# Performance work log

Hardware: AMD Instinct MI355X
Metric: run time of the kernel (lower is better)

Reference implementation:

```python
import jax, jax.numpy as jnp
import numpy as np

B, S, HID = 16, 1024, 768
NH, HD = 12, 64  # num_heads, head_dim


def setup_inputs() -> dict:
    key = jax.random.key(0)
    ks = jax.random.split(key, 10)
    s = 0.02
    return {
        "hidden_states": jax.random.normal(ks[0], (B, S, HID), jnp.float32),
        "channel_importance": jnp.ones((HID,), jnp.float32),
        "context_importance": jnp.ones((HID,), jnp.float32),
        # Linear weights stored as (in, out): y = x @ W + b (== torch x @ W_t.T + b)
        "Wq": jax.random.normal(ks[1], (HID, HID), jnp.float32) * s,
        "bq": jnp.zeros((HID,), jnp.float32),
        "Wk": jax.random.normal(ks[2], (HID, HID), jnp.float32) * s,
        "bk": jnp.zeros((HID,), jnp.float32),
        "Wv": jax.random.normal(ks[3], (HID, HID), jnp.float32) * s,
        "bv": jnp.zeros((HID,), jnp.float32),
        "Wo": jax.random.normal(ks[4], (HID, HID), jnp.float32) * s,
        "bo": jnp.zeros((HID,), jnp.float32),
    }


def reference(hidden_states, channel_importance, context_importance,
              Wq, bq, Wk, bk, Wv, bv, Wo, bo):
    # channel-importance scaling (prune=False branch skipped)
    h = hidden_states * channel_importance  # [B,S,HID]
    # Q/K/V projections, split into heads: [B,S,HID] -> [B,NH,S,HD]
    def heads(x):
        return x.reshape(B, S, NH, HD).transpose(0, 2, 1, 3)
    q = heads(h @ Wq + bq)
    k = heads(h @ Wk + bk)
    v = heads(h @ Wv + bv)
    # scaled dot-product attention (dropout rate 0 -> identity)
    scores = jnp.einsum('bhqd,bhkd->bhqk', q, k) / jnp.sqrt(jnp.float32(HD))
    probs = jax.nn.softmax(scores, axis=-1)
    ctx = jnp.einsum('bhqk,bhkd->bhqd', probs, v)
    ctx = ctx.transpose(0, 2, 1, 3).reshape(B, S, HID)
    # context channel-importance scaling, then output projection
    ctx = ctx * context_importance
    out = ctx @ Wo + bo
    return out  # weights=None since visualize=False
```

## Files before the change

kernel.cpp:

```cpp
#include <hip/hip_runtime.h>
#include <hip/hip_bf16.h>

typedef unsigned short u16;
typedef short bf16x8 __attribute__((ext_vector_type(8)));
typedef float f32x4 __attribute__((ext_vector_type(4)));
typedef float f32x16 __attribute__((ext_vector_type(16)));
typedef unsigned short u16x4 __attribute__((ext_vector_type(4)));
typedef unsigned u32x4 __attribute__((ext_vector_type(4)));

#define SCALE_Q 0.18033688011112042f

__device__ __forceinline__ u16 f2b(float f) {
    __hip_bfloat16 h = __float2bfloat16(f);
    return *reinterpret_cast<u16*>(&h);
}

__device__ __forceinline__ unsigned cvt_pk_bf16(float lo, float hi) {
    unsigned r;
    asm("v_cvt_pk_bf16_f32 %0, %1, %2" : "=v"(r) : "v"(lo), "v"(hi));
    return r;
}

#define hw_exp2 __builtin_amdgcn_exp2f
#define hw_rcp  __builtin_amdgcn_rcpf

__device__ __forceinline__ void load_lds16(const void* g, void* l) {
    __builtin_amdgcn_global_load_lds(
        (const __attribute__((address_space(1))) void*)g,
        (__attribute__((address_space(3))) void*)l, 16, 0, 0);
}

__global__ __launch_bounds__(256) void prep_hidden(
    const float* __restrict__ x, const float* __restrict__ ci, u16* __restrict__ hbuf) {
    size_t i = ((size_t)blockIdx.x * 256 + threadIdx.x) * 4;
    float4 v = *(const float4*)(x + i);
    int c = (int)(i % 768);
    u16x4 o;
    o.x = f2b(v.x * ci[c]);     o.y = f2b(v.y * ci[c + 1]);
    o.z = f2b(v.z * ci[c + 2]); o.w = f2b(v.w * ci[c + 3]);
    *(u16x4*)(hbuf + i) = o;
}

__global__ __launch_bounds__(256) void transpose_w(
    const float* __restrict__ Wq, const float* __restrict__ Wk,
    const float* __restrict__ Wv, const float* __restrict__ Wo,
    const float* __restrict__ cc, u16* __restrict__ wqkvt, u16* __restrict__ wot) {
    __shared__ float tile[32][33];
    int z = blockIdx.z;
    const float* src = (z == 0) ? Wq : (z == 1) ? Wk : (z == 2) ? Wv : Wo;
    u16* dst = (z < 3) ? (wqkvt + (size_t)z * 768 * 768) : wot;
    int tx = threadIdx.x & 31, ty = threadIdx.x >> 5;
    int k0 = blockIdx.x * 32, n0 = blockIdx.y * 32;
    #pragma unroll
    for (int i = ty; i < 32; i += 8) {
        float v = src[(size_t)(k0 + i) * 768 + n0 + tx];
        if (z == 3) v *= cc[k0 + i];
        if (z == 0) v *= SCALE_Q;
        tile[i][tx] = v;
    }
    __syncthreads();
    #pragma unroll
    for (int i = ty; i < 32; i += 8)
        dst[(size_t)(n0 + i) * 768 + k0 + tx] = f2b(tile[tx][i]);
}

__global__ __launch_bounds__(256) void bias_cat(
    const float* __restrict__ bq, const float* __restrict__ bk,
    const float* __restrict__ bv, float* __restrict__ biasq) {
    int i = blockIdx.x * 256 + threadIdx.x;
    biasq[i] = (i < 768) ? bq[i] * SCALE_Q : (i < 1536) ? bk[i - 768] : bv[i - 1536];
}

template <int F32OUT>
__global__ __launch_bounds__(512) void gemm_bt(
    const u16* __restrict__ A, const u16* __restrict__ Bt,
    const float* __restrict__ bias, void* __restrict__ Cout,
    int M, int N, int K, int NTN) {
    __shared__ u16 lds[3 * 24576];
    int nwg = gridDim.x;
    int bid = blockIdx.x;
    int wg = ((nwg & 7) == 0) ? ((bid & 7) * (nwg >> 3) + (bid >> 3)) : bid;
    int mt = wg / NTN, nt = wg % NTN;
    int row0 = mt << 8, col0 = nt << 7;
    int tid = threadIdx.x;
    int lane = tid & 63, wv = tid >> 6;
    int wm = (wv >> 1) << 6;
    int wn = (wv & 1) << 6;
    int l15 = lane & 15, hi = lane >> 4;

    f32x4 acc[4][4] = {};

    auto STAGE = [&](int kt, int s) {
        u16* sl = &lds[s * 24576];
        size_t kof = (size_t)kt << 6;
        #pragma unroll
        for (int p = 0; p < 4; ++p) {
            int c = p * 512 + tid;
            int rr = c >> 3, cc = (c & 7) ^ (rr & 7);
            load_lds16(A + (size_t)(row0 + rr) * K + kof + cc * 8,
                       &sl[(p * 512 + (wv << 6)) << 3]);
        }
        #pragma unroll
        for (int p = 0; p < 2; ++p) {
            int c = p * 512 + tid;
            int rr = c >> 3, cc = (c & 7) ^ (rr & 7);
            load_lds16(Bt + (size_t)(col0 + rr) * K + kof + cc * 8,
                       &sl[16384 + ((p * 512 + (wv << 6)) << 3)]);
        }
    };

    auto COMPUTE = [&](int s) {
        u16* sA = &lds[s * 24576];
        u16* sB = sA + 16384;
        __builtin_amdgcn_s_setprio(1);
        #pragma unroll
        for (int ks = 0; ks < 2; ++ks) {
            bf16x8 af[4], bf[4];
            #pragma unroll
            for (int i = 0; i < 4; ++i) {
                int ra = wm + i * 16 + l15;
                af[i] = *(const bf16x8*)&sA[ra * 64 + (((ks << 2) + hi) ^ (ra & 7)) * 8];
                int rb = wn + i * 16 + l15;
                bf[i] = *(const bf16x8*)&sB[rb * 64 + (((ks << 2) + hi) ^ (rb & 7)) * 8];
            }
            #pragma unroll
            for (int mi = 0; mi < 4; ++mi)
                #pragma unroll
                for (int ni = 0; ni < 4; ++ni)
                    acc[mi][ni] = __builtin_amdgcn_mfma_f32_16x16x32_bf16(
                        af[mi], bf[ni], acc[mi][ni], 0, 0, 0);
        }
        __builtin_amdgcn_s_setprio(0);
    };

    int nkt = K >> 6;
    STAGE(0, 0);
    STAGE(1, 1);

    int s = 0;
    for (int kt = 0; kt < nkt - 2; ++kt) {
        int s2 = s + 2; if (s2 >= 3) s2 -= 3;
        STAGE(kt + 2, s2);
        asm volatile("s_waitcnt vmcnt(12)" ::: "memory");
        __builtin_amdgcn_s_barrier();
        COMPUTE(s);
        asm volatile("s_waitcnt lgkmcnt(0)" ::: "memory");
        __builtin_amdgcn_s_barrier();
        if (++s == 3) s = 0;
    }
    asm volatile("s_waitcnt vmcnt(6)" ::: "memory");
    __builtin_amdgcn_s_barrier();
    COMPUTE(s);
    asm volatile("s_waitcnt lgkmcnt(0)" ::: "memory");
    __builtin_amdgcn_s_barrier();
    if (++s == 3) s = 0;
    asm volatile("s_waitcnt vmcnt(0)" ::: "memory");
    __builtin_amdgcn_s_barrier();
    COMPUTE(s);

    #pragma unroll
    for (int mi = 0; mi < 4; ++mi) {
        int rbase = row0 + wm + mi * 16 + hi * 4;
        #pragma unroll
        for (int ni = 0; ni < 4; ++ni) {
            int c = col0 + wn + ni * 16 + l15;
            float bv = bias[c];
            #pragma unroll
            for (int j = 0; j < 4; ++j) {
                float o = acc[mi][ni][j] + bv;
                if (F32OUT) ((float*)Cout)[(size_t)(rbase + j) * N + c] = o;
                else        ((u16*)Cout)[(size_t)(rbase + j) * N + c] = f2b(o);
            }
        }
    }
}

__global__ __launch_bounds__(512, 4) void attn_kernel(
    const u16* __restrict__ QKV, u16* __restrict__ ctx) {
    __shared__ u16 lK[2][64 * 64];
    __shared__ u16 lV[2][64 * 68];

    int bid = blockIdx.x;
    int wg = (bid & 7) * 96 + (bid >> 3);
    int bh = wg >> 2, qt = wg & 3;
    int b = bh / 12, h = bh % 12;
    int tid = threadIdx.x;
    int lane = tid & 63, wv = tid >> 6;
    int l31 = lane & 31;
    int hb = lane >> 5;

    const u16* Qb = QKV + (size_t)b * 1024 * 2304 + h * 64;
    const u16* Kb = Qb + 768;
    const u16* Vb = Qb + 1536;

    int qrow0 = qt * 256 + wv * 32;

    bf16x8 qf[4];
    #pragma unroll
    for (int ks = 0; ks < 4; ++ks)
        qf[ks] = *(const bf16x8*)(Qb + (size_t)(qrow0 + l31) * 2304 + ks * 16 + hb * 8);

    f32x16 accO0 = {}, accO1 = {};
    float lacc = 0.f;

    int krr = tid >> 3;
    int kcc = (tid & 7) ^ (krr & 7);
    bool vstage = tid < 256;
    int jj0 = (tid & 31) * 2;
    int jjs = (jj0 & ~12) | ((jj0 & 4) << 1) | ((jj0 & 8) >> 1);
    int d0v = ((tid >> 5) & 7) << 3;

    load_lds16(Kb + (size_t)krr * 2304 + kcc * 8, &lK[0][(wv << 6) << 3]);
    if (vstage) {
        bf16x8 g0 = *(const bf16x8*)(Vb + (size_t)jj0 * 2304 + d0v);
        bf16x8 g1 = *(const bf16x8*)(Vb + (size_t)(jj0 + 1) * 2304 + d0v);
        const unsigned* a0 = (const unsigned*)&g0;
        const unsigned* a1 = (const unsigned*)&g1;
        #pragma unroll
        for (int w = 0; w < 4; ++w) {
            *(unsigned*)&lV[0][(d0v + 2 * w) * 68 + jjs] =
                __builtin_amdgcn_perm(a1[w], a0[w], 0x05040100);
            *(unsigned*)&lV[0][(d0v + 2 * w + 1) * 68 + jjs] =
                __builtin_amdgcn_perm(a1[w], a0[w], 0x07060302);
        }
    }
    __syncthreads();

    int cur = 0;
    for (int t = 0; t < 16; ++t) {
        bf16x8 nv0, nv1;
        if (t < 15) {
            size_t kt1 = (size_t)(t + 1) * 64;
            load_lds16(Kb + (kt1 + krr) * 2304 + kcc * 8, &lK[cur ^ 1][(wv << 6) << 3]);
            if (vstage) {
                nv0 = *(const bf16x8*)(Vb + (kt1 + jj0) * 2304 + d0v);
                nv1 = *(const bf16x8*)(Vb + (kt1 + jj0 + 1) * 2304 + d0v);
            }
        }

        #pragma unroll
        for (int kvb = 0; kvb < 2; ++kvb) {
            f32x16 accs = {};
            __builtin_amdgcn_s_setprio(1);
            #pragma unroll
            for (int ks = 0; ks < 4; ++ks) {
                bf16x8 kf = *(const bf16x8*)&lK[cur][
                    (kvb * 32 + l31) * 64 + (((ks << 1) + hb) ^ (l31 & 7)) * 8];
                accs = __builtin_amdgcn_mfma_f32_32x32x16_bf16(kf, qf[ks], accs, 0, 0, 0);
            }
            __builtin_amdgcn_s_setprio(0);

            unsigned W[8];
            float ls = 0.f;
            #pragma unroll
            for (int w = 0; w < 8; ++w) {
                float e0 = hw_exp2(accs[2 * w]);
                float e1 = hw_exp2(accs[2 * w + 1]);
                ls += e0 + e1;
                W[w] = cvt_pk_bf16(e0, e1);
            }
            lacc += ls;

            __builtin_amdgcn_s_setprio(1);
            #pragma unroll
            for (int mm = 0; mm < 2; ++mm) {
                int m = kvb * 2 + mm;
                u32x4 pw;
                pw.x = W[4 * mm];     pw.y = W[4 * mm + 1];
                pw.z = W[4 * mm + 2]; pw.w = W[4 * mm + 3];
                bf16x8 pa = *(bf16x8*)&pw;
                bf16x8 vf0 = *(const bf16x8*)&lV[cur][l31 * 68 + m * 16 + hb * 8];
                bf16x8 vf1 = *(const bf16x8*)&lV[cur][(32 + l31) * 68 + m * 16 + hb * 8];
                accO0 = __builtin_amdgcn_mfma_f32_32x32x16_bf16(pa, vf0, accO0, 0, 0, 0);
                accO1 = __builtin_amdgcn_mfma_f32_32x32x16_bf16(pa, vf1, accO1, 0, 0, 0);
            }
            __builtin_amdgcn_s_setprio(0);
        }

        if (t < 15 && vstage) {
            const unsigned* a0 = (const unsigned*)&nv0;
            const unsigned* a1 = (const unsigned*)&nv1;
            #pragma unroll
            for (int w = 0; w < 4; ++w) {
                *(unsigned*)&lV[cur ^ 1][(d0v + 2 * w) * 68 + jjs] =
                    __builtin_amdgcn_perm(a1[w], a0[w], 0x05040100);
                *(unsigned*)&lV[cur ^ 1][(d0v + 2 * w + 1) * 68 + jjs] =
                    __builtin_amdgcn_perm(a1[w], a0[w], 0x07060302);
            }
        }

        __syncthreads();
        cur ^= 1;
    }

    float lsum = lacc + __shfl_xor(lacc, 32);
    #pragma unroll
    for (int r = 0; r < 16; ++r) {
        int q = (r & 3) + 8 * (r >> 2) + hb * 4;
        float Lr = __shfl(lsum, q);
        float inv = hw_rcp(Lr);
        size_t row = (size_t)(b * 1024 + qrow0 + q);
        ctx[row * 768 + h * 64 + l31]      = f2b(accO0[r] * inv);
        ctx[row * 768 + h * 64 + 32 + l31] = f2b(accO1[r] * inv);
    }
}

extern "C" void kernel_launch(void* const* d_in, const int* in_sizes, int n_in,
                              void* d_out, int out_size, void* d_ws, size_t ws_size,
                              hipStream_t stream) {
    const float* x  = (const float*)d_in[0];
    const float* ci = (const float*)d_in[1];
    const float* cc = (const float*)d_in[2];
    const float* Wq = (const float*)d_in[3];
    const float* bq = (const float*)d_in[4];
    const float* Wk = (const float*)d_in[5];
    const float* bk = (const float*)d_in[6];
    const float* Wv = (const float*)d_in[7];
    const float* bv = (const float*)d_in[8];
    const float* Wo = (const float*)d_in[9];
    const float* bo = (const float*)d_in[10];
    float* out = (float*)d_out;

    unsigned char* ws = (unsigned char*)d_ws;
    size_t off = 0;
    auto alloc = [&](size_t bytes) {
        void* p = ws + off;
        off += (bytes + 255) & ~(size_t)255;
        return p;
    };
    u16*   hbuf  = (u16*)  alloc((size_t)16384 * 768 * 2);
    u16*   wqkvt = (u16*)  alloc((size_t)2304 * 768 * 2);
    u16*   wot   = (u16*)  alloc((size_t)768 * 768 * 2);
    float* biasq = (float*)alloc(2304 * 4);
    u16*   qkv   = (u16*)  alloc((size_t)16384 * 2304 * 2);
    u16*   ctx   = (u16*)  alloc((size_t)16384 * 768 * 2);

    prep_hidden<<<12288, 256, 0, stream>>>(x, ci, hbuf);
    transpose_w<<<dim3(24, 24, 4), 256, 0, stream>>>(Wq, Wk, Wv, Wo, cc, wqkvt, wot);
    bias_cat<<<9, 256, 0, stream>>>(bq, bk, bv, biasq);
    gemm_bt<0><<<1152, 512, 0, stream>>>(hbuf, wqkvt, biasq, qkv, 16384, 2304, 768, 18);
    attn_kernel<<<768, 512, 0, stream>>>(qkv, ctx);
    gemm_bt<1><<<384, 512, 0, stream>>>(ctx, wot, bo, out, 16384, 768, 768, 6);
}
```

Before: 202.3 us.

## Split GEMM k-tile staging and compute into two interleaved phases

The GEMM main loop now splits each k-tile's global-to-LDS staging into two halves and its MFMA compute into two k-sub-phases. Each staging half is issued alongside one compute phase, with a barrier between them. The prologue and epilogue are folded into a single uniform loop with guarded staging and adjusted vmcnt waits. The aim is to spread memory issue across compute and smooth the pipeline, at the cost of an extra barrier per k-tile.

```diff
diff --git a/kernel.cpp b/kernel.cpp
--- a/kernel.cpp
+++ b/kernel.cpp
@@ -90,73 +90,68 @@
 
     f32x4 acc[4][4] = {};
 
-    auto STAGE = [&](int kt, int s) {
+    auto STAGE_PART = [&](int kt, int s, int part) {
         u16* sl = &lds[s * 24576];
         size_t kof = (size_t)kt << 6;
-        #pragma unroll
-        for (int p = 0; p < 4; ++p) {
-            int c = p * 512 + tid;
-            int rr = c >> 3, cc = (c & 7) ^ (rr & 7);
-            load_lds16(A + (size_t)(row0 + rr) * K + kof + cc * 8,
-                       &sl[(p * 512 + (wv << 6)) << 3]);
-        }
+        int pa0 = part * 2;
         #pragma unroll
         for (int p = 0; p < 2; ++p) {
-            int c = p * 512 + tid;
-            int rr = c >> 3, cc = (c & 7) ^ (rr & 7);
-            load_lds16(Bt + (size_t)(col0 + rr) * K + kof + cc * 8,
-                       &sl[16384 + ((p * 512 + (wv << 6)) << 3)]);
+            int c = (pa0 + p) * 512 + tid;
+            int rr = c >> 3, cc2 = (c & 7) ^ (rr & 7);
+            load_lds16(A + (size_t)(row0 + rr) * K + kof + cc2 * 8,
+                       &sl[((pa0 + p) * 512 + (wv << 6)) << 3]);
+        }
+        {
+            int c = part * 512 + tid;
+            int rr = c >> 3, cc2 = (c & 7) ^ (rr & 7);
+            load_lds16(Bt + (size_t)(col0 + rr) * K + kof + cc2 * 8,
+                       &sl[16384 + ((part * 512 + (wv << 6)) << 3)]);
         }
     };
 
-    auto COMPUTE = [&](int s) {
+    auto PHASE = [&](int s, int ks) {
         u16* sA = &lds[s * 24576];
         u16* sB = sA + 16384;
+        bf16x8 af[4], bf[4];
+        #pragma unroll
+        for (int i = 0; i < 4; ++i) {
+            int ra = wm + i * 16 + l15;
+            af[i] = *(const bf16x8*)&sA[ra * 64 + (((ks << 2) + hi) ^ (ra & 7)) * 8];
+            int rb = wn + i * 16 + l15;
+            bf[i] = *(const bf16x8*)&sB[rb * 64 + (((ks << 2) + hi) ^ (rb & 7)) * 8];
+        }
         __builtin_amdgcn_s_setprio(1);
         #pragma unroll
-        for (int ks = 0; ks < 2; ++ks) {
-            bf16x8 af[4], bf[4];
-            #pragma unroll
-            for (int i = 0; i < 4; ++i) {
-                int ra = wm + i * 16 + l15;
-                af[i] = *(const bf16x8*)&sA[ra * 64 + (((ks << 2) + hi) ^ (ra & 7)) * 8];
-                int rb = wn + i * 16 + l15;
-                bf[i] = *(const bf16x8*)&sB[rb * 64 + (((ks << 2) + hi) ^ (rb & 7)) * 8];
-            }
-            #pragma unroll
-            for (int mi = 0; mi < 4; ++mi)
-                #pragma unroll
-                for (int ni = 0; ni < 4; ++ni)
-                    acc[mi][ni] = __builtin_amdgcn_mfma_f32_16x16x32_bf16(
-                        af[mi], bf[ni], acc[mi][ni], 0, 0, 0);
-        }
+        for (int mi = 0; mi < 4; ++mi)
+            #pragma unroll
+            for (int ni = 0; ni < 4; ++ni)
+                acc[mi][ni] = __builtin_amdgcn_mfma_f32_16x16x32_bf16(
+                    af[mi], bf[ni], acc[mi][ni], 0, 0, 0);
         __builtin_amdgcn_s_setprio(0);
     };
 
     int nkt = K >> 6;
-    STAGE(0, 0);
-    STAGE(1, 1);
+    STAGE_PART(0, 0, 0); STAGE_PART(0, 0, 1);
+    STAGE_PART(1, 1, 0); STAGE_PART(1, 1, 1);
+    asm volatile("s_waitcnt vmcnt(6)" ::: "memory");
+    asm volatile("s_barrier" ::: "memory");
 
     int s = 0;
-    for (int kt = 0; kt < nkt - 2; ++kt) {
+    for (int kt = 0; kt < nkt; ++kt) {
         int s2 = s + 2; if (s2 >= 3) s2 -= 3;
-        STAGE(kt + 2, s2);
-        asm volatile("s_waitcnt vmcnt(12)" ::: "memory");
-        __builtin_amdgcn_s_barrier();
-        COMPUTE(s);
+        bool st = kt + 2 < nkt;
+        if (st) STAGE_PART(kt + 2, s2, 0);
+        PHASE(s, 0);
         asm volatile("s_waitcnt lgkmcnt(0)" ::: "memory");
-        __builtin_amdgcn_s_barrier();
+        asm volatile("s_barrier" ::: "memory");
+        if (st) STAGE_PART(kt + 2, s2, 1);
+        PHASE(s, 1);
+        if (st)                  asm volatile("s_waitcnt vmcnt(6)" ::: "memory");
+        else if (kt + 2 == nkt)  asm volatile("s_waitcnt vmcnt(0)" ::: "memory");
+        asm volatile("s_waitcnt lgkmcnt(0)" ::: "memory");
+        asm volatile("s_barrier" ::: "memory");
         if (++s == 3) s = 0;
     }
-    asm volatile("s_waitcnt vmcnt(6)" ::: "memory");
-    __builtin_amdgcn_s_barrier();
-    COMPUTE(s);
-    asm volatile("s_waitcnt lgkmcnt(0)" ::: "memory");
-    __builtin_amdgcn_s_barrier();
-    if (++s == 3) s = 0;
-    asm volatile("s_waitcnt vmcnt(0)" ::: "memory");
-    __builtin_amdgcn_s_barrier();
-    COMPUTE(s);
 
     #pragma unroll
     for (int mi = 0; mi < 4; ++mi) {
```

After: 208.4 us. 1.03x slower.
